# Kernel tuning notes

Hardware: AMD Instinct MI355X
Metric: run time of the kernel (lower is better)

## Reference

```python
import jax, jax.numpy as jnp
import numpy as np

NEG_INF = -1000000000.0
INPUT_SIZE = 1024
HIDDEN_SIZE = 64
B, S = 8, 2048


def setup_inputs() -> dict:
    key = jax.random.key(0)
    ks = jax.random.split(key, 8)
    scale = 1.0 / np.sqrt(INPUT_SIZE)
    inp = {
        "input": jax.random.normal(ks[0], (B, S, INPUT_SIZE), dtype=jnp.float32),
        "mask": jax.random.randint(ks[1], (B, S, S), 0, 2, dtype=jnp.int32),
        "W_q": jax.random.uniform(ks[2], (HIDDEN_SIZE, INPUT_SIZE), jnp.float32, -scale, scale),
        "b_q": jax.random.uniform(ks[3], (HIDDEN_SIZE,), jnp.float32, -scale, scale),
        "W_k": jax.random.uniform(ks[4], (HIDDEN_SIZE, INPUT_SIZE), jnp.float32, -scale, scale),
        "b_k": jax.random.uniform(ks[5], (HIDDEN_SIZE,), jnp.float32, -scale, scale),
        "W_v": jax.random.uniform(ks[6], (HIDDEN_SIZE, INPUT_SIZE), jnp.float32, -scale, scale),
        "b_v": jax.random.uniform(ks[7], (HIDDEN_SIZE,), jnp.float32, -scale, scale),
    }
    return inp


def reference(input, mask, W_q, b_q, W_k, b_k, W_v, b_v):
    inv_sqrt_d = 1.0 / np.sqrt(HIDDEN_SIZE)
    # Q/K/V projections: torch Linear is x @ W.T + b
    q = jnp.einsum('bsi,hi->bsh', input, W_q) + b_q  # (B,S,H)
    k = jnp.einsum('bsi,hi->bsh', input, W_k) + b_k
    v = jnp.einsum('bsi,hi->bsh', input, W_v) + b_v
    scores = jnp.einsum('bqh,bkh->bqk', q, k) * inv_sqrt_d  # (B,S,S)
    scores = jnp.where(mask == 0, NEG_INF, scores)
    probs = jax.nn.softmax(scores, axis=-1)
    return jnp.einsum('bqk,bkh->bqh', probs, v)  # (B,S,H)
```

## Files before the change

kernel.cpp:

```cpp
#include <hip/hip_runtime.h>

typedef __bf16 bf16;
typedef bf16 bf16x4 __attribute__((ext_vector_type(4)));
typedef bf16 bf16x8 __attribute__((ext_vector_type(8)));
typedef float floatx4 __attribute__((ext_vector_type(4)));
typedef unsigned int u32;

#define B_ 8
#define S_ 2048
#define I_ 1024
#define H_ 64
#define NEG_INF_ -1000000000.0f

__device__ __forceinline__ void async_cp16(bf16* lds_base, const bf16* g_base, int lane) {
    __builtin_amdgcn_global_load_lds(
        (const __attribute__((address_space(1))) u32*)(g_base + lane * 8),
        (__attribute__((address_space(3))) u32*)lds_base, 16, 0, 0);
}

__global__ void conv_w(const float* __restrict__ Wq, const float* __restrict__ bq,
                       const float* __restrict__ Wk, const float* __restrict__ bk,
                       const float* __restrict__ Wv, const float* __restrict__ bv,
                       bf16* __restrict__ Wc2, float* __restrict__ bc) {
    int idx = blockIdx.x * 256 + threadIdx.x;
    int n = idx >> 10, i = idx & 1023;
    float v;
    if (n < 64)       v = Wq[n * I_ + i] * 0.125f;
    else if (n < 128) v = Wk[(n - 64) * I_ + i];
    else              v = Wv[(n - 128) * I_ + i];
    int s = i >> 7, kl = i & 127;
    Wc2[(size_t)s * 26112 + n * 136 + kl] = (bf16)v;
    if (idx < 192) {
        float bb = (idx < 64) ? bq[idx] * 0.125f
                 : (idx < 128) ? bk[idx - 64] : bv[idx - 128];
        bc[idx] = bb;
    }
}

__global__ __launch_bounds__(256, 2) void qkv_gemm(const float* __restrict__ X,
                                                   const bf16* __restrict__ Wc2,
                                                   const float* __restrict__ bc,
                                                   bf16* __restrict__ Qd,
                                                   bf16* __restrict__ Kd2,
                                                   bf16* __restrict__ Vt2) {
    __shared__ __align__(16) bf16 Xs[32 * 136];
    __shared__ __align__(16) bf16 Ws[26112];

    int tid = threadIdx.x;
    int w = tid >> 6, lane = tid & 63;
    int n = lane & 15, g = lane >> 4;
    int m0 = blockIdx.x * 32;
    int mt = w & 1, nh = (w >> 1) * 96;

    floatx4 zero4 = {0.0f, 0.0f, 0.0f, 0.0f};
    floatx4 acc[6];
#pragma unroll
    for (int t = 0; t < 6; ++t) acc[t] = zero4;

    int xrow = tid >> 3, xcb = (tid & 7) * 16;
    const float* xsrc = X + (size_t)(m0 + xrow) * I_ + xcb;
    bf16* xdst = Xs + xrow * 136 + xcb;

    for (int s = 0; s < 8; ++s) {
        const float* xp = xsrc + s * 128;
        float4 x0 = *(const float4*)(xp);
        float4 x1 = *(const float4*)(xp + 4);
        float4 x2 = *(const float4*)(xp + 8);
        float4 x3 = *(const float4*)(xp + 12);
#pragma unroll
        for (int i = 0; i < 13; ++i) {
            int inst = i * 4 + w;
            if (inst < 51)
                async_cp16(Ws + inst * 512, Wc2 + (size_t)s * 26112 + inst * 512, lane);
        }
        bf16x8 b0, b1;
        b0[0] = (bf16)x0.x; b0[1] = (bf16)x0.y; b0[2] = (bf16)x0.z; b0[3] = (bf16)x0.w;
        b0[4] = (bf16)x1.x; b0[5] = (bf16)x1.y; b0[6] = (bf16)x1.z; b0[7] = (bf16)x1.w;
        b1[0] = (bf16)x2.x; b1[1] = (bf16)x2.y; b1[2] = (bf16)x2.z; b1[3] = (bf16)x2.w;
        b1[4] = (bf16)x3.x; b1[5] = (bf16)x3.y; b1[6] = (bf16)x3.z; b1[7] = (bf16)x3.w;
        *(bf16x8*)xdst = b0;
        *(bf16x8*)(xdst + 8) = b1;
        __syncthreads();

#pragma unroll
        for (int ks = 0; ks < 4; ++ks) {
            bf16x8 xa = *(bf16x8*)(Xs + (mt * 16 + n) * 136 + ks * 32 + g * 8);
#pragma unroll
            for (int nt = 0; nt < 6; ++nt) {
                bf16x8 wb = *(bf16x8*)(Ws + (nh + nt * 16 + n) * 136 + ks * 32 + g * 8);
                acc[nt] = __builtin_amdgcn_mfma_f32_16x16x32_bf16(xa, wb, acc[nt], 0, 0, 0);
            }
        }
        __syncthreads();
    }

    int b = m0 >> 11;
    int sb = (m0 & 2047) + mt * 16 + g * 4;
#pragma unroll
    for (int nt = 0; nt < 6; ++nt) {
        int ng = nh + nt * 16 + n;
        float bias = bc[ng];
        if (ng < 64) {
#pragma unroll
            for (int r = 0; r < 4; ++r)
                Qd[(size_t)(b * S_ + sb + r) * H_ + ng] = (bf16)(acc[nt][r] + bias);
        } else if (ng < 128) {
            int hc = (ng - 64) >> 3, j = (ng - 64) & 7;
#pragma unroll
            for (int r = 0; r < 4; ++r)
                Kd2[((size_t)(b * 8 + hc) * S_ + sb + r) * 8 + j] = (bf16)(acc[nt][r] + bias);
        } else {
            int hh = ng - 128, kc = sb >> 3, jj = sb & 7;
            bf16x4 pk;
#pragma unroll
            for (int r = 0; r < 4; ++r) pk[r] = (bf16)(acc[nt][r] + bias);
            *(bf16x4*)(Vt2 + ((size_t)(b * 256 + kc) * 64 + hh) * 8 + jj) = pk;
        }
    }
}

__global__ __launch_bounds__(256, 4) void attn(const bf16* __restrict__ Qd,
                                               const bf16* __restrict__ Kd2,
                                               const bf16* __restrict__ Vt2,
                                               const int* __restrict__ mask,
                                               float* __restrict__ po,
                                               float* __restrict__ pml) {
    __shared__ __align__(16) bf16 regA[8704];
    __shared__ __align__(16) bf16 Vs[16 * 528];

    int tid = threadIdx.x;
    int w = tid >> 6, lane = tid & 63;
    int n = lane & 15, g = lane >> 4;
    int bid = blockIdx.x;
    int ksp = bid & 3;
    int qt = (bid >> 2) & 31;
    int b = bid >> 7;
    int q0 = qt * 64;

    const bf16* qptr = Qd + (size_t)(b * S_ + q0 + w * 16 + n) * H_ + g * 8;
    bf16x8 qa0 = *(const bf16x8*)qptr;
    bf16x8 qa1 = *(const bf16x8*)(qptr + 32);

    floatx4 zero4 = {0.0f, 0.0f, 0.0f, 0.0f};
    floatx4 o[4];
#pragma unroll
    for (int t = 0; t < 4; ++t) o[t] = zero4;
    float m_i[4], l_i[4];
#pragma unroll
    for (int r = 0; r < 4; ++r) { m_i[r] = -INFINITY; l_i[r] = 0.0f; }

    for (int kt = ksp * 4; kt < ksp * 4 + 4; ++kt) {
        const int* mb = mask + (size_t)(b * S_ + q0 + w * 16 + g * 4) * S_ + kt * 128 + n;
        int mreg[4][8];
#pragma unroll
        for (int r = 0; r < 4; ++r)
#pragma unroll
            for (int nt = 0; nt < 8; ++nt)
                mreg[r][nt] = mb[(size_t)r * S_ + nt * 16];
#pragma unroll
        for (int j = 0; j < 4; ++j) {
            int hc = w * 2 + (j >> 1), p = j & 1;
            async_cp16(regA + hc * 1040 + p * 512,
                       Kd2 + ((size_t)(b * 8 + hc) * S_ + kt * 128 + p * 64) * 8, lane);
        }
#pragma unroll
        for (int j = 0; j < 4; ++j) {
            int kcl = w * 4 + j;
            async_cp16(Vs + kcl * 528,
                       Vt2 + ((size_t)(b * 256 + kt * 16 + kcl) * 64) * 8, lane);
        }
        __syncthreads();

        floatx4 s[8];
#pragma unroll
        for (int nt = 0; nt < 8; ++nt) {
            floatx4 a = zero4;
            a = __builtin_amdgcn_mfma_f32_16x16x32_bf16(
                    qa0, *(const bf16x8*)(regA + g * 1040 + (nt * 16 + n) * 8), a, 0, 0, 0);
            a = __builtin_amdgcn_mfma_f32_16x16x32_bf16(
                    qa1, *(const bf16x8*)(regA + (4 + g) * 1040 + (nt * 16 + n) * 8), a, 0, 0, 0);
            s[nt] = a;
        }

#pragma unroll
        for (int r = 0; r < 4; ++r)
#pragma unroll
            for (int nt = 0; nt < 8; ++nt)
                if (mreg[r][nt] == 0) s[nt][r] = NEG_INF_;
#pragma unroll
        for (int r = 0; r < 4; ++r) {
            float tm = s[0][r];
#pragma unroll
            for (int nt = 1; nt < 8; ++nt) tm = fmaxf(tm, s[nt][r]);
#pragma unroll
            for (int off = 1; off < 16; off <<= 1) tm = fmaxf(tm, __shfl_xor(tm, off, 64));
            float mn = fmaxf(m_i[r], tm);
            float alpha = __expf(m_i[r] - mn);
            m_i[r] = mn;
            float rs = 0.0f;
#pragma unroll
            for (int nt = 0; nt < 8; ++nt) {
                float p = __expf(s[nt][r] - mn);
                s[nt][r] = p;
                rs += p;
            }
#pragma unroll
            for (int off = 1; off < 16; off <<= 1) rs += __shfl_xor(rs, off, 64);
            l_i[r] = l_i[r] * alpha + rs;
#pragma unroll
            for (int ht = 0; ht < 4; ++ht) o[ht][r] *= alpha;
        }
        __syncthreads();

#pragma unroll
        for (int r = 0; r < 4; ++r)
#pragma unroll
            for (int nt = 0; nt < 8; ++nt)
                regA[(w * 16 + g * 4 + r) * 136 + nt * 16 + n] = (bf16)s[nt][r];
        __syncthreads();

#pragma unroll
        for (int k0 = 0; k0 < 4; ++k0) {
            bf16x8 pa = *(bf16x8*)(regA + (w * 16 + n) * 136 + k0 * 32 + g * 8);
#pragma unroll
            for (int ht = 0; ht < 4; ++ht) {
                bf16x8 vb = *(bf16x8*)(Vs + (k0 * 4 + g) * 528 + (ht * 16 + n) * 8);
                o[ht] = __builtin_amdgcn_mfma_f32_16x16x32_bf16(pa, vb, o[ht], 0, 0, 0);
            }
        }
        __syncthreads();
    }

    float* pb = po + (size_t)bid * 4096;
#pragma unroll
    for (int ht = 0; ht < 4; ++ht)
#pragma unroll
        for (int r = 0; r < 4; ++r)
            pb[(w * 16 + g * 4 + r) * 64 + ht * 16 + n] = o[ht][r];
    if (n == 0) {
#pragma unroll
        for (int r = 0; r < 4; ++r) {
            pml[(size_t)bid * 128 + w * 16 + g * 4 + r] = m_i[r];
            pml[(size_t)bid * 128 + 64 + w * 16 + g * 4 + r] = l_i[r];
        }
    }
}

__global__ __launch_bounds__(256) void reduce_o(const float* __restrict__ po,
                                                const float* __restrict__ pml,
                                                float* __restrict__ out) {
    int idx = blockIdx.x * 256 + threadIdx.x;
    int h = idx & 63, q = idx >> 6;
    int b = q >> 11, qq = q & 2047;
    int qt = qq >> 6, ql = qq & 63;
    int bid0 = (b * 32 + qt) * 4;
    float mj[4], lj[4], M = -INFINITY;
#pragma unroll
    for (int j = 0; j < 4; ++j) {
        mj[j] = pml[(size_t)(bid0 + j) * 128 + ql];
        lj[j] = pml[(size_t)(bid0 + j) * 128 + 64 + ql];
        M = fmaxf(M, mj[j]);
    }
    float num = 0.0f, den = 0.0f;
#pragma unroll
    for (int j = 0; j < 4; ++j) {
        float sc = __expf(mj[j] - M);
        den += lj[j] * sc;
        num += po[(size_t)(bid0 + j) * 4096 + ql * 64 + h] * sc;
    }
    out[(size_t)q * 64 + h] = num / den;
}

extern "C" void kernel_launch(void* const* d_in, const int* in_sizes, int n_in,
                              void* d_out, int out_size, void* d_ws, size_t ws_size,
                              hipStream_t stream) {
    const float* X    = (const float*)d_in[0];
    const int*   mask = (const int*)d_in[1];
    const float* Wq   = (const float*)d_in[2];
    const float* bq   = (const float*)d_in[3];
    const float* Wk   = (const float*)d_in[4];
    const float* bk   = (const float*)d_in[5];
    const float* Wv   = (const float*)d_in[6];
    const float* bv   = (const float*)d_in[7];
    float* out = (float*)d_out;

    char* p = (char*)d_ws;
    bf16* Qd   = (bf16*)p;  p += (size_t)B_ * S_ * H_ * 2;
    bf16* Kd2  = (bf16*)p;  p += (size_t)B_ * S_ * H_ * 2;
    bf16* Vt2  = (bf16*)p;  p += (size_t)B_ * S_ * H_ * 2;
    bf16* Wc2  = (bf16*)p;  p += (size_t)8 * 26112 * 2;
    float* bc  = (float*)p; p += 1024;
    float* po  = (float*)p; p += (size_t)1024 * 4096 * 4;
    float* pml = (float*)p; p += (size_t)1024 * 128 * 4;

    conv_w<<<dim3(768), dim3(256), 0, stream>>>(Wq, bq, Wk, bk, Wv, bv, Wc2, bc);
    qkv_gemm<<<dim3(512), dim3(256), 0, stream>>>(X, Wc2, bc, Qd, Kd2, Vt2);
    attn<<<dim3(1024), dim3(256), 0, stream>>>(Qd, Kd2, Vt2, mask, po, pml);
    reduce_o<<<dim3(4096), dim3(256), 0, stream>>>(po, pml, out);
}
```

Measured before the change: 266.3 us.

## Double-buffer K/V and prefetch mask in attention; pipeline X loads in QKV GEMM

The attention kernel now uses 512-thread blocks covering 128 query rows with a 2-way key split instead of 4-way. K and V tiles are double-buffered in LDS and the next tile's mask values are prefetched into registers, with explicit vmcnt/lgkmcnt waits replacing most __syncthreads. This is meant to hide global latency on the mask and K/V loads and to halve the partial-output traffic seen by the reduce kernel. In exchange the grid drops to 256 blocks, so occupancy is lower. The QKV GEMM also prefetches the next X slice into registers and drops the copy guard, so the last weight slice over-reads a little past its end.

```diff
diff --git a/kernel.cpp b/kernel.cpp
--- a/kernel.cpp
+++ b/kernel.cpp
@@ -16,6 +16,22 @@
     __builtin_amdgcn_global_load_lds(
         (const __attribute__((address_space(1))) u32*)(g_base + lane * 8),
         (__attribute__((address_space(3))) u32*)lds_base, 16, 0, 0);
+}
+
+template<int N> __device__ __forceinline__ void wait_vm() {
+    asm volatile("s_waitcnt vmcnt(%0)" :: "n"(N) : "memory");
+}
+__device__ __forceinline__ void wait_lgkm0() {
+    asm volatile("s_waitcnt lgkmcnt(0)" ::: "memory");
+}
+__device__ __forceinline__ void barrier_() {
+    asm volatile("" ::: "memory");
+    __builtin_amdgcn_s_barrier();
+    asm volatile("" ::: "memory");
+}
+__device__ __forceinline__ void fence_order() {
+    __builtin_amdgcn_sched_barrier(0);
+    asm volatile("" ::: "memory");
 }
 
 __global__ void conv_w(const float* __restrict__ Wq, const float* __restrict__ bq,
@@ -44,7 +60,7 @@
                                                    bf16* __restrict__ Kd2,
                                                    bf16* __restrict__ Vt2) {
     __shared__ __align__(16) bf16 Xs[32 * 136];
-    __shared__ __align__(16) bf16 Ws[26112];
+    __shared__ __align__(16) bf16 Ws[26624];
 
     int tid = threadIdx.x;
     int w = tid >> 6, lane = tid & 63;
@@ -61,37 +77,49 @@
     const float* xsrc = X + (size_t)(m0 + xrow) * I_ + xcb;
     bf16* xdst = Xs + xrow * 136 + xcb;
 
+    float4 xa = *(const float4*)(xsrc);
+    float4 xb = *(const float4*)(xsrc + 4);
+    float4 xc = *(const float4*)(xsrc + 8);
+    float4 xd = *(const float4*)(xsrc + 12);
+
     for (int s = 0; s < 8; ++s) {
-        const float* xp = xsrc + s * 128;
-        float4 x0 = *(const float4*)(xp);
-        float4 x1 = *(const float4*)(xp + 4);
-        float4 x2 = *(const float4*)(xp + 8);
-        float4 x3 = *(const float4*)(xp + 12);
 #pragma unroll
         for (int i = 0; i < 13; ++i) {
             int inst = i * 4 + w;
-            if (inst < 51)
-                async_cp16(Ws + inst * 512, Wc2 + (size_t)s * 26112 + inst * 512, lane);
+            async_cp16(Ws + inst * 512, Wc2 + (size_t)s * 26112 + inst * 512, lane);
         }
         bf16x8 b0, b1;
-        b0[0] = (bf16)x0.x; b0[1] = (bf16)x0.y; b0[2] = (bf16)x0.z; b0[3] = (bf16)x0.w;
-        b0[4] = (bf16)x1.x; b0[5] = (bf16)x1.y; b0[6] = (bf16)x1.z; b0[7] = (bf16)x1.w;
-        b1[0] = (bf16)x2.x; b1[1] = (bf16)x2.y; b1[2] = (bf16)x2.z; b1[3] = (bf16)x2.w;
-        b1[4] = (bf16)x3.x; b1[5] = (bf16)x3.y; b1[6] = (bf16)x3.z; b1[7] = (bf16)x3.w;
+        b0[0] = (bf16)xa.x; b0[1] = (bf16)xa.y; b0[2] = (bf16)xa.z; b0[3] = (bf16)xa.w;
+        b0[4] = (bf16)xb.x; b0[5] = (bf16)xb.y; b0[6] = (bf16)xb.z; b0[7] = (bf16)xb.w;
+        b1[0] = (bf16)xc.x; b1[1] = (bf16)xc.y; b1[2] = (bf16)xc.z; b1[3] = (bf16)xc.w;
+        b1[4] = (bf16)xd.x; b1[5] = (bf16)xd.y; b1[6] = (bf16)xd.z; b1[7] = (bf16)xd.w;
         *(bf16x8*)xdst = b0;
         *(bf16x8*)(xdst + 8) = b1;
-        __syncthreads();
+        fence_order();
+        if (s < 7) {
+            const float* xp = xsrc + (s + 1) * 128;
+            xa = *(const float4*)(xp);
+            xb = *(const float4*)(xp + 4);
+            xc = *(const float4*)(xp + 8);
+            xd = *(const float4*)(xp + 12);
+            wait_vm<4>();
+        } else {
+            wait_vm<0>();
+        }
+        wait_lgkm0();
+        barrier_();
 
 #pragma unroll
         for (int ks = 0; ks < 4; ++ks) {
-            bf16x8 xa = *(bf16x8*)(Xs + (mt * 16 + n) * 136 + ks * 32 + g * 8);
+            bf16x8 xv = *(bf16x8*)(Xs + (mt * 16 + n) * 136 + ks * 32 + g * 8);
 #pragma unroll
             for (int nt = 0; nt < 6; ++nt) {
                 bf16x8 wb = *(bf16x8*)(Ws + (nh + nt * 16 + n) * 136 + ks * 32 + g * 8);
-                acc[nt] = __builtin_amdgcn_mfma_f32_16x16x32_bf16(xa, wb, acc[nt], 0, 0, 0);
+                acc[nt] = __builtin_amdgcn_mfma_f32_16x16x32_bf16(xv, wb, acc[nt], 0, 0, 0);
             }
         }
-        __syncthreads();
+        wait_lgkm0();
+        barrier_();
     }
 
     int b = m0 >> 11;
@@ -119,23 +147,24 @@
     }
 }
 
-__global__ __launch_bounds__(256, 4) void attn(const bf16* __restrict__ Qd,
+__global__ __launch_bounds__(512, 2) void attn(const bf16* __restrict__ Qd,
                                                const bf16* __restrict__ Kd2,
                                                const bf16* __restrict__ Vt2,
                                                const int* __restrict__ mask,
                                                float* __restrict__ po,
                                                float* __restrict__ pml) {
-    __shared__ __align__(16) bf16 regA[8704];
-    __shared__ __align__(16) bf16 Vs[16 * 528];
+    __shared__ __align__(16) bf16 Ks[2][8 * 1040];
+    __shared__ __align__(16) bf16 Vs[2][16 * 528];
+    __shared__ __align__(16) bf16 Ps[128 * 136];
 
     int tid = threadIdx.x;
     int w = tid >> 6, lane = tid & 63;
     int n = lane & 15, g = lane >> 4;
     int bid = blockIdx.x;
-    int ksp = bid & 3;
-    int qt = (bid >> 2) & 31;
-    int b = bid >> 7;
-    int q0 = qt * 64;
+    int ksp = bid & 1;
+    int qt = (bid >> 1) & 15;
+    int b = bid >> 5;
+    int q0 = qt * 128;
 
     const bf16* qptr = Qd + (size_t)(b * S_ + q0 + w * 16 + n) * H_ + g * 8;
     bf16x8 qa0 = *(const bf16x8*)qptr;
@@ -149,89 +178,128 @@
 #pragma unroll
     for (int r = 0; r < 4; ++r) { m_i[r] = -INFINITY; l_i[r] = 0.0f; }
 
-    for (int kt = ksp * 4; kt < ksp * 4 + 4; ++kt) {
-        const int* mb = mask + (size_t)(b * S_ + q0 + w * 16 + g * 4) * S_ + kt * 128 + n;
-        int mreg[4][8];
+    int kt0 = ksp * 8;
+    const int* mbase = mask + (size_t)(b * S_ + q0 + w * 16 + g * 4) * S_ + n;
+    int mreg[4][8];
+
+    {
+        async_cp16(&Ks[0][w * 1040],       Kd2 + ((size_t)(b * 8 + w) * S_ + kt0 * 128) * 8, lane);
+        async_cp16(&Ks[0][w * 1040 + 512], Kd2 + ((size_t)(b * 8 + w) * S_ + kt0 * 128 + 64) * 8, lane);
+        async_cp16(&Vs[0][(w * 2) * 528],     Vt2 + ((size_t)(b * 256 + kt0 * 16 + w * 2) * 64) * 8, lane);
+        async_cp16(&Vs[0][(w * 2 + 1) * 528], Vt2 + ((size_t)(b * 256 + kt0 * 16 + w * 2 + 1) * 64) * 8, lane);
+        fence_order();
+        const int* mb = mbase + (size_t)kt0 * S_ * 0 + (size_t)kt0 * 128;
 #pragma unroll
         for (int r = 0; r < 4; ++r)
 #pragma unroll
             for (int nt = 0; nt < 8; ++nt)
                 mreg[r][nt] = mb[(size_t)r * S_ + nt * 16];
-#pragma unroll
-        for (int j = 0; j < 4; ++j) {
-            int hc = w * 2 + (j >> 1), p = j & 1;
-            async_cp16(regA + hc * 1040 + p * 512,
-                       Kd2 + ((size_t)(b * 8 + hc) * S_ + kt * 128 + p * 64) * 8, lane);
-        }
-#pragma unroll
-        for (int j = 0; j < 4; ++j) {
-            int kcl = w * 4 + j;
-            async_cp16(Vs + kcl * 528,
-                       Vt2 + ((size_t)(b * 256 + kt * 16 + kcl) * 64) * 8, lane);
-        }
-        __syncthreads();
+    }
+
+#pragma unroll 2
+    for (int it = 0; it < 8; ++it) {
+        int kt = kt0 + it;
+        int cur = it & 1;
+        bf16* ksc = &Ks[cur][0];
+        bf16* vsc = &Vs[cur][0];
+
+        wait_vm<32>();
+        wait_lgkm0();
+        barrier_();
+
+        if (it < 7) {
+            int nxt = cur ^ 1;
+            async_cp16(&Ks[nxt][w * 1040],       Kd2 + ((size_t)(b * 8 + w) * S_ + (kt + 1) * 128) * 8, lane);
+            async_cp16(&Ks[nxt][w * 1040 + 512], Kd2 + ((size_t)(b * 8 + w) * S_ + (kt + 1) * 128 + 64) * 8, lane);
+            async_cp16(&Vs[nxt][(w * 2) * 528],     Vt2 + ((size_t)(b * 256 + (kt + 1) * 16 + w * 2) * 64) * 8, lane);
+            async_cp16(&Vs[nxt][(w * 2 + 1) * 528], Vt2 + ((size_t)(b * 256 + (kt + 1) * 16 + w * 2 + 1) * 64) * 8, lane);
+        }
 
         floatx4 s[8];
 #pragma unroll
         for (int nt = 0; nt < 8; ++nt) {
             floatx4 a = zero4;
             a = __builtin_amdgcn_mfma_f32_16x16x32_bf16(
-                    qa0, *(const bf16x8*)(regA + g * 1040 + (nt * 16 + n) * 8), a, 0, 0, 0);
+                    qa0, *(const bf16x8*)(ksc + g * 1040 + (nt * 16 + n) * 8), a, 0, 0, 0);
             a = __builtin_amdgcn_mfma_f32_16x16x32_bf16(
-                    qa1, *(const bf16x8*)(regA + (4 + g) * 1040 + (nt * 16 + n) * 8), a, 0, 0, 0);
+                    qa1, *(const bf16x8*)(ksc + (4 + g) * 1040 + (nt * 16 + n) * 8), a, 0, 0, 0);
             s[nt] = a;
         }
 
+        if (it < 7) wait_vm<4>(); else wait_vm<0>();
 #pragma unroll
         for (int r = 0; r < 4; ++r)
 #pragma unroll
             for (int nt = 0; nt < 8; ++nt)
                 if (mreg[r][nt] == 0) s[nt][r] = NEG_INF_;
+
+        if (it < 7) {
+            const int* mb = mbase + (size_t)(kt + 1) * 128;
+#pragma unroll
+            for (int r = 0; r < 4; ++r)
+#pragma unroll
+                for (int nt = 0; nt < 8; ++nt)
+                    mreg[r][nt] = mb[(size_t)r * S_ + nt * 16];
+        }
+
+        float tm[4];
 #pragma unroll
         for (int r = 0; r < 4; ++r) {
-            float tm = s[0][r];
-#pragma unroll
-            for (int nt = 1; nt < 8; ++nt) tm = fmaxf(tm, s[nt][r]);
-#pragma unroll
-            for (int off = 1; off < 16; off <<= 1) tm = fmaxf(tm, __shfl_xor(tm, off, 64));
-            float mn = fmaxf(m_i[r], tm);
-            float alpha = __expf(m_i[r] - mn);
+            float t = s[0][r];
+#pragma unroll
+            for (int nt = 1; nt < 8; ++nt) t = fmaxf(t, s[nt][r]);
+            tm[r] = t;
+        }
+#pragma unroll
+        for (int off = 1; off < 16; off <<= 1)
+#pragma unroll
+            for (int r = 0; r < 4; ++r) tm[r] = fmaxf(tm[r], __shfl_xor(tm[r], off, 64));
+        float alpha[4], rs[4];
+#pragma unroll
+        for (int r = 0; r < 4; ++r) {
+            float mn = fmaxf(m_i[r], tm[r]);
+            alpha[r] = __expf(m_i[r] - mn);
             m_i[r] = mn;
-            float rs = 0.0f;
+            rs[r] = 0.0f;
+        }
+#pragma unroll
+        for (int r = 0; r < 4; ++r)
 #pragma unroll
             for (int nt = 0; nt < 8; ++nt) {
-                float p = __expf(s[nt][r] - mn);
+                float p = __expf(s[nt][r] - m_i[r]);
                 s[nt][r] = p;
-                rs += p;
+                rs[r] += p;
             }
 #pragma unroll
-            for (int off = 1; off < 16; off <<= 1) rs += __shfl_xor(rs, off, 64);
-            l_i[r] = l_i[r] * alpha + rs;
-#pragma unroll
-            for (int ht = 0; ht < 4; ++ht) o[ht][r] *= alpha;
-        }
-        __syncthreads();
+        for (int off = 1; off < 16; off <<= 1)
+#pragma unroll
+            for (int r = 0; r < 4; ++r) rs[r] += __shfl_xor(rs[r], off, 64);
+#pragma unroll
+        for (int r = 0; r < 4; ++r) {
+            l_i[r] = l_i[r] * alpha[r] + rs[r];
+#pragma unroll
+            for (int ht = 0; ht < 4; ++ht) o[ht][r] *= alpha[r];
+        }
 
 #pragma unroll
         for (int r = 0; r < 4; ++r)
 #pragma unroll
             for (int nt = 0; nt < 8; ++nt)
-                regA[(w * 16 + g * 4 + r) * 136 + nt * 16 + n] = (bf16)s[nt][r];
-        __syncthreads();
+                Ps[(w * 16 + g * 4 + r) * 136 + nt * 16 + n] = (bf16)s[nt][r];
+        wait_lgkm0();
 
 #pragma unroll
         for (int k0 = 0; k0 < 4; ++k0) {
-            bf16x8 pa = *(bf16x8*)(regA + (w * 16 + n) * 136 + k0 * 32 + g * 8);
+            bf16x8 pa = *(bf16x8*)(Ps + (w * 16 + n) * 136 + k0 * 32 + g * 8);
 #pragma unroll
             for (int ht = 0; ht < 4; ++ht) {
-                bf16x8 vb = *(bf16x8*)(Vs + (k0 * 4 + g) * 528 + (ht * 16 + n) * 8);
+                bf16x8 vb = *(bf16x8*)(vsc + (k0 * 4 + g) * 528 + (ht * 16 + n) * 8);
                 o[ht] = __builtin_amdgcn_mfma_f32_16x16x32_bf16(pa, vb, o[ht], 0, 0, 0);
             }
         }
-        __syncthreads();
-    }
-
-    float* pb = po + (size_t)bid * 4096;
+    }
+
+    float* pb = po + (size_t)bid * 8192;
 #pragma unroll
     for (int ht = 0; ht < 4; ++ht)
 #pragma unroll
@@ -240,8 +308,8 @@
     if (n == 0) {
 #pragma unroll
         for (int r = 0; r < 4; ++r) {
-            pml[(size_t)bid * 128 + w * 16 + g * 4 + r] = m_i[r];
-            pml[(size_t)bid * 128 + 64 + w * 16 + g * 4 + r] = l_i[r];
+            pml[(size_t)bid * 256 + w * 16 + g * 4 + r] = m_i[r];
+            pml[(size_t)bid * 256 + 128 + w * 16 + g * 4 + r] = l_i[r];
         }
     }
 }
@@ -252,22 +320,17 @@
     int idx = blockIdx.x * 256 + threadIdx.x;
     int h = idx & 63, q = idx >> 6;
     int b = q >> 11, qq = q & 2047;
-    int qt = qq >> 6, ql = qq & 63;
-    int bid0 = (b * 32 + qt) * 4;
-    float mj[4], lj[4], M = -INFINITY;
-#pragma unroll
-    for (int j = 0; j < 4; ++j) {
-        mj[j] = pml[(size_t)(bid0 + j) * 128 + ql];
-        lj[j] = pml[(size_t)(bid0 + j) * 128 + 64 + ql];
-        M = fmaxf(M, mj[j]);
-    }
-    float num = 0.0f, den = 0.0f;
-#pragma unroll
-    for (int j = 0; j < 4; ++j) {
-        float sc = __expf(mj[j] - M);
-        den += lj[j] * sc;
-        num += po[(size_t)(bid0 + j) * 4096 + ql * 64 + h] * sc;
-    }
+    int qt = qq >> 7, ql = qq & 127;
+    int bid0 = (b * 16 + qt) * 2;
+    float m0 = pml[(size_t)bid0 * 256 + ql];
+    float l0 = pml[(size_t)bid0 * 256 + 128 + ql];
+    float m1 = pml[(size_t)(bid0 + 1) * 256 + ql];
+    float l1 = pml[(size_t)(bid0 + 1) * 256 + 128 + ql];
+    float M = fmaxf(m0, m1);
+    float s0 = __expf(m0 - M), s1 = __expf(m1 - M);
+    float den = l0 * s0 + l1 * s1;
+    float num = po[(size_t)bid0 * 8192 + ql * 64 + h] * s0
+              + po[(size_t)(bid0 + 1) * 8192 + ql * 64 + h] * s1;
     out[(size_t)q * 64 + h] = num / den;
 }
 
@@ -290,11 +353,11 @@
     bf16* Vt2  = (bf16*)p;  p += (size_t)B_ * S_ * H_ * 2;
     bf16* Wc2  = (bf16*)p;  p += (size_t)8 * 26112 * 2;
     float* bc  = (float*)p; p += 1024;
-    float* po  = (float*)p; p += (size_t)1024 * 4096 * 4;
-    float* pml = (float*)p; p += (size_t)1024 * 128 * 4;
+    float* po  = (float*)p; p += (size_t)512 * 8192 * 4;
+    float* pml = (float*)p; p += (size_t)512 * 256 * 4;
 
     conv_w<<<dim3(768), dim3(256), 0, stream>>>(Wq, bq, Wk, bk, Wv, bv, Wc2, bc);
     qkv_gemm<<<dim3(512), dim3(256), 0, stream>>>(X, Wc2, bc, Qd, Kd2, Vt2);
-    attn<<<dim3(1024), dim3(256), 0, stream>>>(Qd, Kd2, Vt2, mask, po, pml);
+    attn<<<dim3(256), dim3(512), 0, stream>>>(Qd, Kd2, Vt2, mask, po, pml);
     reduce_o<<<dim3(4096), dim3(256), 0, stream>>>(po, pml, out);
 }
```

Result: no change. 265.6 us (-0.3%).
